# Optimization experiments

Measured on AMD Instinct MI355X. Metric: run time of the kernel, lower is better.

Reference implementation:

```python
import jax, jax.numpy as jnp
import numpy as np

N_QUBITS = 8
N_CYCLES = 4
N_LAYERS = 2  # log2(8) - 1
B = 65536

CNOT = jnp.array([[1, 0, 0, 0],
                  [0, 1, 0, 0],
                  [0, 0, 0, 1],
                  [0, 0, 1, 0]], dtype=jnp.complex64)


def apply_gate(state, U, wires):
    """Apply a (2^k x 2^k) gate U on the given wires of state (B, 2,2,...,2).
    Wire 0 is the leftmost (most significant) qubit axis."""
    k = len(wires)
    src = [w + 1 for w in wires]
    dst = list(range(1, 1 + k))
    st = jnp.moveaxis(state, src, dst)
    shp = st.shape
    st = st.reshape(shp[0], 2 ** k, -1)
    st = jnp.einsum('ij,bjr->bir', U, st)
    return jnp.moveaxis(st.reshape(shp), dst, src)


def apply_ry(state, q, angles):
    """Batched RY(angle) on qubit q; angles has shape (B,)."""
    st = jnp.moveaxis(state, q + 1, 1)  # (B, 2, rest...)
    c = jnp.cos(0.5 * angles).reshape((-1,) + (1,) * (st.ndim - 2))
    s = jnp.sin(0.5 * angles).reshape((-1,) + (1,) * (st.ndim - 2))
    s0, s1 = st[:, 0], st[:, 1]
    new = jnp.stack([c * s0 - s * s1, s * s0 + c * s1], axis=1)
    return jnp.moveaxis(new, 1, q + 1)


def crx_mat(theta):
    c = (jnp.cos(0.5 * theta) + 0j).astype(jnp.complex64)
    s = (-1j * jnp.sin(0.5 * theta)).astype(jnp.complex64)
    one = jnp.ones((), jnp.complex64)
    zero = jnp.zeros((), jnp.complex64)
    return jnp.stack([
        jnp.stack([one, zero, zero, zero]),
        jnp.stack([zero, one, zero, zero]),
        jnp.stack([zero, zero, c, s]),
        jnp.stack([zero, zero, s, c]),
    ])


def u3_mat(p):
    th, ph, lm = p[0], p[1], p[2]
    ct = (jnp.cos(0.5 * th) + 0j).astype(jnp.complex64)
    st = (jnp.sin(0.5 * th) + 0j).astype(jnp.complex64)
    el = jnp.exp(1j * lm).astype(jnp.complex64)
    ep = jnp.exp(1j * ph).astype(jnp.complex64)
    return jnp.stack([
        jnp.stack([ct, -el * st]),
        jnp.stack([ep * st, ep * el * ct]),
    ])


def expval_z(state, q):
    st = jnp.moveaxis(state, q + 1, 1)
    p = (st.real ** 2 + st.imag ** 2).reshape(st.shape[0], 2, -1).sum(-1)
    return p[:, 0] - p[:, 1]


def _forward(x, crx_theta, u3_params, w1, b1, w2, b2):
    b = x.shape[0]
    # |0...0> initial state, shape (B, 2,2,...,2)
    state = jnp.zeros((b, 2 ** N_QUBITS), jnp.complex64).at[:, 0].set(1.0)
    state = state.reshape((b,) + (2,) * N_QUBITS)
    # encoder: data re-uploading RY angle encoding + CNOT ring, n_cycles times
    for _ in range(N_CYCLES):
        for q in range(N_QUBITS):
            state = apply_ry(state, q, x[:, q])
        for q in range(N_QUBITS):
            state = apply_gate(state, CNOT, [q, (q + 1) % N_QUBITS])
    # QCNN conv/pool layers with shared weights per layer
    active = list(range(N_QUBITS))
    for layer in range(N_LAYERS):
        U = crx_mat(crx_theta[layer])
        for i in range(0, len(active) - 1, 2):
            state = apply_gate(state, U, [active[i], active[i + 1]])
        for i in range(1, len(active) - 1, 2):
            state = apply_gate(state, U, [active[i], active[i + 1]])
        remain = active[1::2]
        # mid-circuit expval in the original is discarded and does not alter state
        V = u3_mat(u3_params[layer])
        for q in remain:
            state = apply_gate(state, V, [q])
        active = remain
    feats = jnp.stack([expval_z(state, q) for q in active], axis=1)  # (B, 2)
    h = jnp.tanh(feats @ w1 + b1)
    return jax.nn.sigmoid(h @ w2 + b2)  # (B, 1)


def setup_inputs() -> dict:
    key = jax.random.key(0)
    ks = jax.random.split(key, 6)
    return {
        'x': jax.random.normal(ks[0], (B, N_QUBITS), jnp.float32),
        'crx_theta': jax.random.normal(ks[1], (N_LAYERS,), jnp.float32),
        'u3_params': jax.random.normal(ks[2], (N_LAYERS, 3), jnp.float32),
        'w1': jax.random.normal(ks[3], (2, 10), jnp.float32) * 0.5,
        'b1': jnp.zeros((10,), jnp.float32),
        'w2': jax.random.normal(ks[4], (10, 1), jnp.float32) * 0.5,
        'b2': jnp.zeros((1,), jnp.float32),
    }


def reference(x, crx_theta, u3_params, w1, b1, w2, b2):
    return _forward(x, crx_theta, u3_params, w1, b1, w2, b2)
```

## Files before the change

### kernel.cpp

```cpp
#include <hip/hip_runtime.h>


#define NQ 8
#define NE 2
typedef _Float16 h2 __attribute__((ext_vector_type(2)));

__device__ __forceinline__ float h2f(h2 v){ return __builtin_bit_cast(float, v); }
__device__ __forceinline__ h2 f2h(float v){ return __builtin_bit_cast(h2, v); }
__device__ __forceinline__ h2 u2h(unsigned u){ return __builtin_bit_cast(h2, u); }
__device__ __forceinline__ unsigned h2u(h2 v){ return __builtin_bit_cast(unsigned, v); }
__device__ __forceinline__ h2 negh(h2 v){ return u2h(h2u(v) ^ 0x80008000u); }
__device__ __forceinline__ h2 mk(float x){ return __builtin_bit_cast(h2, __builtin_amdgcn_cvt_pkrtz(x,x)); }
__device__ __forceinline__ h2 mk2(float a, float b){ return __builtin_bit_cast(h2, __builtin_amdgcn_cvt_pkrtz(a,b)); }
__device__ __forceinline__ h2 fma2h(h2 a, h2 b, h2 c){ return __builtin_elementwise_fma(a,b,c); }
__device__ __forceinline__ h2 swp(h2 v){ return __builtin_shufflevector(v,v,1,0); }
__device__ __forceinline__ h2 permh(h2 a, h2 b, unsigned sel){
    return u2h(__builtin_amdgcn_perm(h2u(a), h2u(b), sel));
}

template<int CTRL>
__device__ __forceinline__ float dppf(float v){
    return __int_as_float(__builtin_amdgcn_mov_dpp(__float_as_int(v), CTRL, 0xF, 0xF, true));
}
template<int M>
__device__ __forceinline__ float sx(float v){
    if constexpr (M==1)       return dppf<0xB1>(v);
    else if constexpr (M==2)  return dppf<0x4E>(v);
    else if constexpr (M==32) return __shfl_xor(v, 32, 64);
    else return __int_as_float(__builtin_amdgcn_ds_swizzle(__float_as_int(v), (M<<10)|0x1F));
}
__device__ __forceinline__ void cmulh(h2&R, h2&I, h2 C, h2 S, h2 nS){
    h2 nR = fma2h(C, R, nS*I);
    I = fma2h(C, I, S*R);
    R = nR;
}

#define FOR_E _Pragma("unroll") for (int e = 0; e < NE; ++e)

__global__ void qcnn_prep(const float* __restrict__ crx,
                          const float* __restrict__ u3p,
                          unsigned* __restrict__ ws){
    if (threadIdx.x==0 && blockIdx.x==0){
        auto PK=[](float lo, float hi)->unsigned{
            unsigned a=__builtin_bit_cast(unsigned short,(_Float16)lo);
            unsigned b=__builtin_bit_cast(unsigned short,(_Float16)hi);
            return a | (b<<16);
        };
        float sc0,cc0,sc1,cc1;
        __sincosf(0.5f*crx[0],&sc0,&cc0);
        __sincosf(0.5f*crx[1],&sc1,&cc1);
        ws[0]=PK(cc0,cc0); ws[1]=PK(sc0,sc0); ws[2]=PK(cc1,cc1); ws[3]=PK(sc1,sc1);
        float th0=u3p[0], ph0=u3p[1], lm0=u3p[2];
        float ust0,uct0; __sincosf(0.5f*th0,&ust0,&uct0);
        ws[4]=PK(uct0,uct0); ws[5]=PK(ust0,ust0); ws[6]=PK(-ust0,-ust0); ws[7]=PK(-ust0,ust0);
        float th1=u3p[3], ph1=u3p[4], lm1=u3p[5];
        float ust1,uct1; __sincosf(0.5f*th1,&ust1,&uct1);
        float sl1,cl1;   __sincosf(lm1,&sl1,&cl1);
        float sp1,cp1;   __sincosf(ph1,&sp1,&cp1);
        ws[8]=PK(uct1,uct1); ws[9]=PK(ust1,ust1); ws[10]=PK(-ust1,-ust1);
        ws[11]=PK(cl1,cl1); ws[12]=PK(sl1,sl1); ws[13]=PK(cp1,cp1); ws[14]=PK(sp1,sp1);
        float cpl1=cp1*cl1-sp1*sl1, spl1=sp1*cl1+cp1*sl1;
        float u01r=-ust1*cl1, u01i=-ust1*sl1;
        float u10r= ust1*cp1, u10i= ust1*sp1;
        float u11r= uct1*cpl1, u11i= uct1*spl1;
        ws[15]=PK(uct1,u11r); ws[16]=PK(u01r,u10r); ws[17]=PK(0.f,-u11i);
        ws[18]=PK(-u01i,-u10i); ws[19]=PK(0.f,u11i); ws[20]=PK(u01i,u10i);
        for(int k=0;k<4;++k){
            float kf=(float)k, sA,cA,sB,cB,sA2,cA2,sB2,cB2;
            __sincosf(lm0*kf,      &sA,&cA);
            __sincosf(lm0*(kf+1.f),&sB,&cB);
            __sincosf(ph0*kf,      &sA2,&cA2);
            __sincosf(ph0*(kf+1.f),&sB2,&cB2);
            unsigned* q = ws + 24 + k*4;
            q[0]=PK(cA,cB); q[1]=PK(sA,sB); q[2]=PK(cA2,cB2); q[3]=PK(sA2,sB2);
        }
    }
}

__global__ __launch_bounds__(256) void qcnn_kernel(
    const float* __restrict__ x,
    const unsigned* __restrict__ wsu,
    const float* __restrict__ w1,
    const float* __restrict__ b1,
    const float* __restrict__ w2,
    const float* __restrict__ b2,
    float* __restrict__ out,
    int Btot)
{
    const int gtid = blockIdx.x*256 + threadIdx.x;
    const int wv = gtid >> 6;
    const int l = threadIdx.x & 63;
    const int e0 = wv * NE;
    if (e0 >= Btot) return;
    const bool L5=(l>>5)&1, L4=(l>>4)&1, L3=(l>>3)&1, L2=(l>>2)&1, L1=(l>>1)&1, L0=l&1;

    const bool pb = __builtin_popcount(l) & 1;
    const int ba0 = (((l&32)|((l^(l>>1))&31)) << 2);
    const int ba1 = ba0 ^ (48<<2);

    const bool bits[6]={L5,L4,L3,L2,L1,L0};
    unsigned sm[6];
#pragma unroll
    for(int q=0;q<6;++q) sm[q] = bits[q] ? 0u : 0x80008000u;

    h2 cH[NE][6], tsH[NE][6];
    h2 c6h[NE], s6h[NE], ns6h[NE], c7h[NE], sv7h[NE];
    h2 A[NE], B[NE];
    FOR_E {
        const float4* xv = (const float4*)(x + (e0+e)*NQ);
        float4 xa=xv[0], xb=xv[1];
        float ang[8]={xa.x,xa.y,xa.z,xa.w,xb.x,xb.y,xb.z,xb.w};
        float cq[8], sq[8];
#pragma unroll
        for(int q=0;q<8;++q) __sincosf(0.5f*ang[q], &sq[q], &cq[q]);
#pragma unroll
        for(int q=0;q<6;++q){
            cH[e][q]=mk(cq[q]);
            tsH[e][q]=u2h(h2u(mk(sq[q])) ^ sm[q]);
        }
        c6h[e]=mk(cq[6]); s6h[e]=mk(sq[6]); ns6h[e]=negh(s6h[e]);
        c7h[e]=mk(cq[7]); sv7h[e]=mk2(-sq[7], sq[7]);
        float pl = (L5?sq[0]:cq[0])*(L4?sq[1]:cq[1])*(L3?sq[2]:cq[2])
                 * (L2?sq[3]:cq[3])*(L1?sq[4]:cq[4])*(L0?sq[5]:cq[5]);
        float pc6=pl*cq[6], ps6=pl*sq[6];
        A[e] = mk2(pc6*cq[7], pc6*sq[7]);
        B[e] = mk2(ps6*cq[7], ps6*sq[7]);
    }

    const h2 cc0h=u2h(wsu[0]), sn0h=u2h(wsu[1]), cc1h=u2h(wsu[2]), sn1h=u2h(wsu[3]);
    const h2 nsn0h=negh(sn0h), nsn1h=negh(sn1h);
    const h2 uct0h=u2h(wsu[4]), ust0h=u2h(wsu[5]), nust0h=u2h(wsu[6]), usv0h=u2h(wsu[7]);
    const h2 uct1h=u2h(wsu[8]), ust1h=u2h(wsu[9]), nust1h=u2h(wsu[10]);
    const h2 cl1h=u2h(wsu[11]), sl1h=u2h(wsu[12]), nsl1h=negh(sl1h);
    const h2 cp1h=u2h(wsu[13]), sp1h=u2h(wsu[14]), nsp1h=negh(sp1h);
    const h2 E0h=u2h(wsu[15]), E1h=u2h(wsu[16]), E2h=u2h(wsu[17]);
    const h2 E3h=u2h(wsu[18]), G2h=u2h(wsu[19]), G3h=u2h(wsu[20]);
    const int ki = (int)L4 + (int)L2 + (int)L0;
    uint4 dt = *(const uint4*)(wsu + 24 + ki*4);
    const h2 Clm=u2h(dt.x), Slm=u2h(dt.y), Cph=u2h(dt.z), Sph=u2h(dt.w);
    const h2 nSlm=negh(Slm), nSph=negh(Sph);
    const h2 tu1H = L4 ? ust0h : nust0h;
    const h2 tu3H = L2 ? ust0h : nust0h;
    const h2 tu5H = L0 ? ust0h : nust0h;

#define RY_L(q, M) do { FOR_E { \
    h2 oA = f2h(sx<M>(h2f(A[e]))), oB = f2h(sx<M>(h2f(B[e]))); \
    A[e] = fma2h(cH[e][q], A[e], tsH[e][q]*oA); \
    B[e] = fma2h(cH[e][q], B[e], tsH[e][q]*oB); } \
} while(0)

#define RINGF() do { FOR_E { \
    h2 TA = pb ? B[e] : A[e]; \
    h2 TS = pb ? A[e] : B[e]; \
    int V0 = (int)__builtin_amdgcn_perm(h2u(TS), h2u(TA), 0x07060100u); \
    int V1 = (int)__builtin_amdgcn_perm(h2u(TA), h2u(TS), 0x07060100u); \
    unsigned r0 = (unsigned)__builtin_amdgcn_ds_bpermute(ba0, V0); \
    unsigned r1 = (unsigned)__builtin_amdgcn_ds_bpermute(ba1, V1); \
    A[e] = u2h(__builtin_amdgcn_perm(r1, r0, 0x07060100u)); \
    B[e] = u2h(__builtin_amdgcn_perm(r1, r0, 0x05040302u)); } \
} while(0)

    RINGF();
#pragma unroll
    for(int cyc=0;cyc<3;++cyc){
        RY_L(0,32); RY_L(1,16); RY_L(2,8); RY_L(3,4); RY_L(4,2); RY_L(5,1);
        FOR_E { h2 nA = fma2h(c6h[e], A[e], ns6h[e]*B[e]);
                h2 nB = fma2h(s6h[e], A[e], c6h[e]*B[e]);
                A[e]=nA; B[e]=nB; }
        FOR_E { A[e] = fma2h(c7h[e], A[e], sv7h[e]*swp(A[e]));
                B[e] = fma2h(c7h[e], B[e], sv7h[e]*swp(B[e])); }
        RINGF();
    }

    h2 RA[NE], RB[NE], IA[NE], IB[NE];
    FOR_E { RA[e]=A[e]; RB[e]=B[e]; IA[e]=(h2){0,0}; IB[e]=(h2){0,0}; }

#define SHF4(M) h2 oRA[NE], oIA[NE], oRB[NE], oIB[NE]; \
    FOR_E { oRA[e]=f2h(sx<M>(h2f(RA[e]))); oIA[e]=f2h(sx<M>(h2f(IA[e]))); \
            oRB[e]=f2h(sx<M>(h2f(RB[e]))); oIB[e]=f2h(sx<M>(h2f(IB[e]))); }
#define CRX_LL(CSH, M, cc, sn, nsn) do { \
    const bool ct = (l >> (CSH)) & 1; \
    SHF4(M) \
    if (ct) { FOR_E { \
        RA[e] = fma2h(cc, RA[e], (sn)*oIA[e]); IA[e] = fma2h(cc, IA[e], (nsn)*oRA[e]); \
        RB[e] = fma2h(cc, RB[e], (sn)*oIB[e]); IB[e] = fma2h(cc, IB[e], (nsn)*oRB[e]); } } \
} while(0)
#define RYC0(M, T) do { \
    SHF4(M) \
    FOR_E { \
    RA[e] = fma2h(uct0h, RA[e], (T)*oRA[e]); IA[e] = fma2h(uct0h, IA[e], (T)*oIA[e]); \
    RB[e] = fma2h(uct0h, RB[e], (T)*oRB[e]); IB[e] = fma2h(uct0h, IB[e], (T)*oIB[e]); } \
} while(0)

    {   h2 oA[NE], oB[NE];
        FOR_E { oA[e]=f2h(sx<16>(h2f(RA[e]))); oB[e]=f2h(sx<16>(h2f(RB[e]))); }
        if (L5){ FOR_E {
            IA[e] = nsn0h*oA[e]; RA[e] = cc0h*RA[e];
            IB[e] = nsn0h*oB[e]; RB[e] = cc0h*RB[e]; } }
    }
    CRX_LL(3, 4, cc0h, sn0h, nsn0h);
    CRX_LL(1, 1, cc0h, sn0h, nsn0h);
    FOR_E {
        h2 oI = swp(IB[e]), oR = swp(RB[e]);
        RB[e] = fma2h(cc0h, RB[e], sn0h*oI);
        IB[e] = fma2h(cc0h, IB[e], nsn0h*oR);
    }
    CRX_LL(4, 8, cc0h, sn0h, nsn0h);
    CRX_LL(2, 2, cc0h, sn0h, nsn0h);
    if (L0) { FOR_E {
        h2 nRA = fma2h(cc0h, RA[e], sn0h*IB[e]);
        h2 nRB = fma2h(cc0h, RB[e], sn0h*IA[e]);
        h2 nIA = fma2h(cc0h, IA[e], nsn0h*RB[e]);
        h2 nIB = fma2h(cc0h, IB[e], nsn0h*RA[e]);
        RA[e]=nRA; RB[e]=nRB; IA[e]=nIA; IB[e]=nIB; } }
    FOR_E { cmulh(RA[e],IA[e],Clm,Slm,nSlm); cmulh(RB[e],IB[e],Clm,Slm,nSlm); }
    RYC0(16, tu1H);
    RYC0(4,  tu3H);
    RYC0(1,  tu5H);
    FOR_E {
        h2 sA=swp(RA[e]), sB=swp(RB[e]), tA=swp(IA[e]), tB=swp(IB[e]);
        RA[e] = fma2h(uct0h, RA[e], usv0h*sA); RB[e] = fma2h(uct0h, RB[e], usv0h*sB);
        IA[e] = fma2h(uct0h, IA[e], usv0h*tA); IB[e] = fma2h(uct0h, IB[e], usv0h*tB);
    }
    FOR_E { cmulh(RA[e],IA[e],Cph,Sph,nSph); cmulh(RB[e],IB[e],Cph,Sph,nSph); }

    CRX_LL(4, 4, cc1h, sn1h, nsn1h);
    if (L0) { FOR_E {
        h2 sIA=swp(IA[e]), sRA=swp(RA[e]), sIB=swp(IB[e]), sRB=swp(RB[e]);
        RA[e] = fma2h(cc1h, RA[e], sn1h*sIA); IA[e] = fma2h(cc1h, IA[e], nsn1h*sRA);
        RB[e] = fma2h(cc1h, RB[e], sn1h*sIB); IB[e] = fma2h(cc1h, IB[e], nsn1h*sRB); } }
    CRX_LL(2, 1, cc1h, sn1h, nsn1h);
    {
        if (L2){ FOR_E { cmulh(RA[e],IA[e],cl1h,sl1h,nsl1h); cmulh(RB[e],IB[e],cl1h,sl1h,nsl1h); } }
        h2 T = L2 ? ust1h : nust1h;
        SHF4(4)
        FOR_E {
            RA[e] = fma2h(uct1h, RA[e], T*oRA[e]); IA[e] = fma2h(uct1h, IA[e], T*oIA[e]);
            RB[e] = fma2h(uct1h, RB[e], T*oRB[e]); IB[e] = fma2h(uct1h, IB[e], T*oIB[e]);
        }
        if (L2){ FOR_E { cmulh(RA[e],IA[e],cp1h,sp1h,nsp1h); cmulh(RB[e],IB[e],cp1h,sp1h,nsp1h); } }
    }
    FOR_E {
        h2 sR=swp(RA[e]), sI=swp(IA[e]);
        h2 nR = fma2h(E3h,sI, fma2h(E2h,IA[e], fma2h(E1h,sR, E0h*RA[e])));
        h2 nI = fma2h(G3h,sR, fma2h(G2h,RA[e], fma2h(E1h,sI, E0h*IA[e])));
        RA[e]=nR; IA[e]=nI;
        h2 sR2=swp(RB[e]), sI2=swp(IB[e]);
        h2 nR2 = fma2h(E3h,sI2, fma2h(E2h,IB[e], fma2h(E1h,sR2, E0h*RB[e])));
        h2 nI2 = fma2h(G3h,sR2, fma2h(G2h,RB[e], fma2h(E1h,sI2, E0h*IB[e])));
        RB[e]=nR2; IB[e]=nI2;
    }

    float f0[NE], f1[NE];
    FOR_E {
        h2 P0 = permh(IA[e], RA[e], 0x05040100u);
        h2 P1 = permh(IA[e], RA[e], 0x07060302u);
        h2 P2 = permh(IB[e], RB[e], 0x05040100u);
        h2 P3 = permh(IB[e], RB[e], 0x07060302u);
        float q02 = __builtin_amdgcn_fdot2(P0, P0,
                      __builtin_amdgcn_fdot2(P2, P2, 0.0f, false), false);
        float q13 = __builtin_amdgcn_fdot2(P1, P1,
                      __builtin_amdgcn_fdot2(P3, P3, 0.0f, false), false);
        float tot = q02 + q13;
        f0[e] = L2 ? -tot : tot;
        f1[e] = q02 - q13;
    }

#define ROUTED_REDUCE(F, OUTV) do { \
    float u = L5 ? F[1] : F[0]; \
    float w = L5 ? F[0] : F[1]; \
    u += sx<32>(w); \
    u += sx<16>(u); u += sx<8>(u); u += sx<4>(u); u += sx<2>(u); u += sx<1>(u); \
    OUTV = u; \
} while(0)

    float F0, F1;
    ROUTED_REDUCE(f0, F0);
    ROUTED_REDUCE(f1, F1);

    const int k = l & 15;
    float contrib = 0.0f;
    if (k < 10) {
        float z = fmaf(F0, w1[k], fmaf(F1, w1[10+k], b1[k]));
        float ex = __expf(2.0f*z);
        contrib = ((ex-1.0f)/(ex+1.0f)) * w2[k];
    }
    contrib += sx<1>(contrib);
    contrib += sx<2>(contrib);
    contrib += sx<4>(contrib);
    contrib += sx<8>(contrib);
    if ((l & 31) == 0) {
        float a = contrib + b2[0];
        out[e0 + (l>>5)] = 1.0f/(1.0f + __expf(-a));
    }
}

extern "C" void kernel_launch(void* const* d_in, const int* in_sizes, int n_in,
                              void* d_out, int out_size, void* d_ws, size_t ws_size,
                              hipStream_t stream) {
    const float* x   = (const float*)d_in[0];
    const float* crx = (const float*)d_in[1];
    const float* u3p = (const float*)d_in[2];
    const float* w1  = (const float*)d_in[3];
    const float* b1  = (const float*)d_in[4];
    const float* w2  = (const float*)d_in[5];
    const float* b2  = (const float*)d_in[6];
    float* out = (float*)d_out;
    unsigned* ws = (unsigned*)d_ws;

    const int B = in_sizes[0] / NQ;
    hipLaunchKernelGGL(qcnn_prep, dim3(1), dim3(64), 0, stream, crx, u3p, ws);
    const int waves = (B + NE - 1) / NE;
    const int wavesPerBlock = 4;
    const int grid = (waves + wavesPerBlock - 1) / wavesPerBlock;
    hipLaunchKernelGGL(qcnn_kernel, dim3(grid), dim3(256), 0, stream,
                       x, ws, w1, b1, w2, b2, out, B);
}
```

Before: 117.5 us.

## Precompute data-independent second phase as unitary and apply via MFMA

The second circuit phase (CRX/U3 layers) does not depend on the input, so a prep kernel builds its 256x256 complex unitary by pushing basis states through it, then a second kernel repacks it into MFMA B-fragments. The main kernel runs the input-dependent RY/CRX cycles per element, stages the states in swizzled LDS, and multiplies them by the unitary with fp16 16x16x32 MFMAs, then reduces the Z expectations through shared memory. Blocks grow to 1024 threads covering 32 elements. This replaces the per-element shuffle-heavy gate sequence with a dense matmul, at the cost of two extra launches, a large workspace read, and more arithmetic per element.

```diff
diff --git a/kernel.cpp b/kernel.cpp
--- a/kernel.cpp
+++ b/kernel.cpp
@@ -3,7 +3,13 @@
 
 #define NQ 8
 #define NE 2
+#define FRAG_OFF 0
+#define UR_OFF   65536
+#define UI_OFF   98304
+
 typedef _Float16 h2 __attribute__((ext_vector_type(2)));
+typedef _Float16 h8 __attribute__((ext_vector_type(8)));
+typedef float    f4 __attribute__((ext_vector_type(4)));
 
 __device__ __forceinline__ float h2f(h2 v){ return __builtin_bit_cast(float, v); }
 __device__ __forceinline__ h2 f2h(float v){ return __builtin_bit_cast(h2, v); }
@@ -14,9 +20,6 @@
 __device__ __forceinline__ h2 mk2(float a, float b){ return __builtin_bit_cast(h2, __builtin_amdgcn_cvt_pkrtz(a,b)); }
 __device__ __forceinline__ h2 fma2h(h2 a, h2 b, h2 c){ return __builtin_elementwise_fma(a,b,c); }
 __device__ __forceinline__ h2 swp(h2 v){ return __builtin_shufflevector(v,v,1,0); }
-__device__ __forceinline__ h2 permh(h2 a, h2 b, unsigned sel){
-    return u2h(__builtin_amdgcn_perm(h2u(a), h2u(b), sel));
-}
 
 template<int CTRL>
 __device__ __forceinline__ float dppf(float v){
@@ -29,6 +32,9 @@
     else if constexpr (M==32) return __shfl_xor(v, 32, 64);
     else return __int_as_float(__builtin_amdgcn_ds_swizzle(__float_as_int(v), (M<<10)|0x1F));
 }
+__device__ __forceinline__ float bperm(int ba, float v){
+    return __int_as_float(__builtin_amdgcn_ds_bpermute(ba, __float_as_int(v)));
+}
 __device__ __forceinline__ void cmulh(h2&R, h2&I, h2 C, h2 S, h2 nS){
     h2 nR = fma2h(C, R, nS*I);
     I = fma2h(C, I, S*R);
@@ -36,118 +42,6 @@
 }
 
 #define FOR_E _Pragma("unroll") for (int e = 0; e < NE; ++e)
-
-__global__ void qcnn_prep(const float* __restrict__ crx,
-                          const float* __restrict__ u3p,
-                          unsigned* __restrict__ ws){
-    if (threadIdx.x==0 && blockIdx.x==0){
-        auto PK=[](float lo, float hi)->unsigned{
-            unsigned a=__builtin_bit_cast(unsigned short,(_Float16)lo);
-            unsigned b=__builtin_bit_cast(unsigned short,(_Float16)hi);
-            return a | (b<<16);
-        };
-        float sc0,cc0,sc1,cc1;
-        __sincosf(0.5f*crx[0],&sc0,&cc0);
-        __sincosf(0.5f*crx[1],&sc1,&cc1);
-        ws[0]=PK(cc0,cc0); ws[1]=PK(sc0,sc0); ws[2]=PK(cc1,cc1); ws[3]=PK(sc1,sc1);
-        float th0=u3p[0], ph0=u3p[1], lm0=u3p[2];
-        float ust0,uct0; __sincosf(0.5f*th0,&ust0,&uct0);
-        ws[4]=PK(uct0,uct0); ws[5]=PK(ust0,ust0); ws[6]=PK(-ust0,-ust0); ws[7]=PK(-ust0,ust0);
-        float th1=u3p[3], ph1=u3p[4], lm1=u3p[5];
-        float ust1,uct1; __sincosf(0.5f*th1,&ust1,&uct1);
-        float sl1,cl1;   __sincosf(lm1,&sl1,&cl1);
-        float sp1,cp1;   __sincosf(ph1,&sp1,&cp1);
-        ws[8]=PK(uct1,uct1); ws[9]=PK(ust1,ust1); ws[10]=PK(-ust1,-ust1);
-        ws[11]=PK(cl1,cl1); ws[12]=PK(sl1,sl1); ws[13]=PK(cp1,cp1); ws[14]=PK(sp1,sp1);
-        float cpl1=cp1*cl1-sp1*sl1, spl1=sp1*cl1+cp1*sl1;
-        float u01r=-ust1*cl1, u01i=-ust1*sl1;
-        float u10r= ust1*cp1, u10i= ust1*sp1;
-        float u11r= uct1*cpl1, u11i= uct1*spl1;
-        ws[15]=PK(uct1,u11r); ws[16]=PK(u01r,u10r); ws[17]=PK(0.f,-u11i);
-        ws[18]=PK(-u01i,-u10i); ws[19]=PK(0.f,u11i); ws[20]=PK(u01i,u10i);
-        for(int k=0;k<4;++k){
-            float kf=(float)k, sA,cA,sB,cB,sA2,cA2,sB2,cB2;
-            __sincosf(lm0*kf,      &sA,&cA);
-            __sincosf(lm0*(kf+1.f),&sB,&cB);
-            __sincosf(ph0*kf,      &sA2,&cA2);
-            __sincosf(ph0*(kf+1.f),&sB2,&cB2);
-            unsigned* q = ws + 24 + k*4;
-            q[0]=PK(cA,cB); q[1]=PK(sA,sB); q[2]=PK(cA2,cB2); q[3]=PK(sA2,sB2);
-        }
-    }
-}
-
-__global__ __launch_bounds__(256) void qcnn_kernel(
-    const float* __restrict__ x,
-    const unsigned* __restrict__ wsu,
-    const float* __restrict__ w1,
-    const float* __restrict__ b1,
-    const float* __restrict__ w2,
-    const float* __restrict__ b2,
-    float* __restrict__ out,
-    int Btot)
-{
-    const int gtid = blockIdx.x*256 + threadIdx.x;
-    const int wv = gtid >> 6;
-    const int l = threadIdx.x & 63;
-    const int e0 = wv * NE;
-    if (e0 >= Btot) return;
-    const bool L5=(l>>5)&1, L4=(l>>4)&1, L3=(l>>3)&1, L2=(l>>2)&1, L1=(l>>1)&1, L0=l&1;
-
-    const bool pb = __builtin_popcount(l) & 1;
-    const int ba0 = (((l&32)|((l^(l>>1))&31)) << 2);
-    const int ba1 = ba0 ^ (48<<2);
-
-    const bool bits[6]={L5,L4,L3,L2,L1,L0};
-    unsigned sm[6];
-#pragma unroll
-    for(int q=0;q<6;++q) sm[q] = bits[q] ? 0u : 0x80008000u;
-
-    h2 cH[NE][6], tsH[NE][6];
-    h2 c6h[NE], s6h[NE], ns6h[NE], c7h[NE], sv7h[NE];
-    h2 A[NE], B[NE];
-    FOR_E {
-        const float4* xv = (const float4*)(x + (e0+e)*NQ);
-        float4 xa=xv[0], xb=xv[1];
-        float ang[8]={xa.x,xa.y,xa.z,xa.w,xb.x,xb.y,xb.z,xb.w};
-        float cq[8], sq[8];
-#pragma unroll
-        for(int q=0;q<8;++q) __sincosf(0.5f*ang[q], &sq[q], &cq[q]);
-#pragma unroll
-        for(int q=0;q<6;++q){
-            cH[e][q]=mk(cq[q]);
-            tsH[e][q]=u2h(h2u(mk(sq[q])) ^ sm[q]);
-        }
-        c6h[e]=mk(cq[6]); s6h[e]=mk(sq[6]); ns6h[e]=negh(s6h[e]);
-        c7h[e]=mk(cq[7]); sv7h[e]=mk2(-sq[7], sq[7]);
-        float pl = (L5?sq[0]:cq[0])*(L4?sq[1]:cq[1])*(L3?sq[2]:cq[2])
-                 * (L2?sq[3]:cq[3])*(L1?sq[4]:cq[4])*(L0?sq[5]:cq[5]);
-        float pc6=pl*cq[6], ps6=pl*sq[6];
-        A[e] = mk2(pc6*cq[7], pc6*sq[7]);
-        B[e] = mk2(ps6*cq[7], ps6*sq[7]);
-    }
-
-    const h2 cc0h=u2h(wsu[0]), sn0h=u2h(wsu[1]), cc1h=u2h(wsu[2]), sn1h=u2h(wsu[3]);
-    const h2 nsn0h=negh(sn0h), nsn1h=negh(sn1h);
-    const h2 uct0h=u2h(wsu[4]), ust0h=u2h(wsu[5]), nust0h=u2h(wsu[6]), usv0h=u2h(wsu[7]);
-    const h2 uct1h=u2h(wsu[8]), ust1h=u2h(wsu[9]), nust1h=u2h(wsu[10]);
-    const h2 cl1h=u2h(wsu[11]), sl1h=u2h(wsu[12]), nsl1h=negh(sl1h);
-    const h2 cp1h=u2h(wsu[13]), sp1h=u2h(wsu[14]), nsp1h=negh(sp1h);
-    const h2 E0h=u2h(wsu[15]), E1h=u2h(wsu[16]), E2h=u2h(wsu[17]);
-    const h2 E3h=u2h(wsu[18]), G2h=u2h(wsu[19]), G3h=u2h(wsu[20]);
-    const int ki = (int)L4 + (int)L2 + (int)L0;
-    uint4 dt = *(const uint4*)(wsu + 24 + ki*4);
-    const h2 Clm=u2h(dt.x), Slm=u2h(dt.y), Cph=u2h(dt.z), Sph=u2h(dt.w);
-    const h2 nSlm=negh(Slm), nSph=negh(Sph);
-    const h2 tu1H = L4 ? ust0h : nust0h;
-    const h2 tu3H = L2 ? ust0h : nust0h;
-    const h2 tu5H = L0 ? ust0h : nust0h;
-
-#define RY_L(q, M) do { FOR_E { \
-    h2 oA = f2h(sx<M>(h2f(A[e]))), oB = f2h(sx<M>(h2f(B[e]))); \
-    A[e] = fma2h(cH[e][q], A[e], tsH[e][q]*oA); \
-    B[e] = fma2h(cH[e][q], B[e], tsH[e][q]*oB); } \
-} while(0)
 
 #define RINGF() do { FOR_E { \
     h2 TA = pb ? B[e] : A[e]; \
@@ -160,20 +54,36 @@
     B[e] = u2h(__builtin_amdgcn_perm(r1, r0, 0x05040302u)); } \
 } while(0)
 
-    RINGF();
-#pragma unroll
-    for(int cyc=0;cyc<3;++cyc){
-        RY_L(0,32); RY_L(1,16); RY_L(2,8); RY_L(3,4); RY_L(4,2); RY_L(5,1);
-        FOR_E { h2 nA = fma2h(c6h[e], A[e], ns6h[e]*B[e]);
-                h2 nB = fma2h(s6h[e], A[e], c6h[e]*B[e]);
-                A[e]=nA; B[e]=nB; }
-        FOR_E { A[e] = fma2h(c7h[e], A[e], sv7h[e]*swp(A[e]));
-                B[e] = fma2h(c7h[e], B[e], sv7h[e]*swp(B[e])); }
-        RINGF();
-    }
-
-    h2 RA[NE], RB[NE], IA[NE], IB[NE];
-    FOR_E { RA[e]=A[e]; RB[e]=B[e]; IA[e]=(h2){0,0}; IB[e]=(h2){0,0}; }
+struct P2C {
+    h2 cc0,sn0,nsn0, cc1,sn1,nsn1;
+    h2 uct0,ust0,nust0,usv0;
+    h2 uct1,ust1,nust1;
+    h2 cl1,sl1,nsl1, cp1,sp1,nsp1;
+    h2 E0,E1,E2,E3,G2,G3;
+    h2 Clm,Slm,nSlm,Cph,Sph,nSph;
+    h2 tu1,tu3,tu5;
+};
+
+__device__ __forceinline__ P2C load_consts(const unsigned* wsu, int l){
+    P2C K;
+    const bool L4=(l>>4)&1, L2=(l>>2)&1, L0=l&1;
+    K.cc0=u2h(wsu[0]); K.sn0=u2h(wsu[1]); K.cc1=u2h(wsu[2]); K.sn1=u2h(wsu[3]);
+    K.nsn0=negh(K.sn0); K.nsn1=negh(K.sn1);
+    K.uct0=u2h(wsu[4]); K.ust0=u2h(wsu[5]); K.nust0=u2h(wsu[6]); K.usv0=u2h(wsu[7]);
+    K.uct1=u2h(wsu[8]); K.ust1=u2h(wsu[9]); K.nust1=u2h(wsu[10]);
+    K.cl1=u2h(wsu[11]); K.sl1=u2h(wsu[12]); K.nsl1=negh(K.sl1);
+    K.cp1=u2h(wsu[13]); K.sp1=u2h(wsu[14]); K.nsp1=negh(K.sp1);
+    K.E0=u2h(wsu[15]); K.E1=u2h(wsu[16]); K.E2=u2h(wsu[17]);
+    K.E3=u2h(wsu[18]); K.G2=u2h(wsu[19]); K.G3=u2h(wsu[20]);
+    const int ki = (int)L4 + (int)L2 + (int)L0;
+    K.Clm=u2h(wsu[24+ki*4+0]); K.Slm=u2h(wsu[24+ki*4+1]);
+    K.Cph=u2h(wsu[24+ki*4+2]); K.Sph=u2h(wsu[24+ki*4+3]);
+    K.nSlm=negh(K.Slm); K.nSph=negh(K.Sph);
+    K.tu1 = L4 ? K.ust0 : K.nust0;
+    K.tu3 = L2 ? K.ust0 : K.nust0;
+    K.tu5 = L0 ? K.ust0 : K.nust0;
+    return K;
+}
 
 #define SHF4(M) h2 oRA[NE], oIA[NE], oRB[NE], oIB[NE]; \
     FOR_E { oRA[e]=f2h(sx<M>(h2f(RA[e]))); oIA[e]=f2h(sx<M>(h2f(IA[e]))); \
@@ -188,110 +98,315 @@
 #define RYC0(M, T) do { \
     SHF4(M) \
     FOR_E { \
-    RA[e] = fma2h(uct0h, RA[e], (T)*oRA[e]); IA[e] = fma2h(uct0h, IA[e], (T)*oIA[e]); \
-    RB[e] = fma2h(uct0h, RB[e], (T)*oRB[e]); IB[e] = fma2h(uct0h, IB[e], (T)*oIB[e]); } \
+    RA[e] = fma2h(K.uct0, RA[e], (T)*oRA[e]); IA[e] = fma2h(K.uct0, IA[e], (T)*oIA[e]); \
+    RB[e] = fma2h(K.uct0, RB[e], (T)*oRB[e]); IB[e] = fma2h(K.uct0, IB[e], (T)*oIB[e]); } \
 } while(0)
+
+__device__ __forceinline__ void phase2run(const int l, const P2C& K,
+    const h2* A, const h2* B, h2* RA, h2* RB, h2* IA, h2* IB)
+{
+    const bool L5=(l>>5)&1, L2=(l>>2)&1, L0=l&1;
+    FOR_E { RA[e]=A[e]; RB[e]=B[e]; IA[e]=(h2){0,0}; IB[e]=(h2){0,0}; }
 
     {   h2 oA[NE], oB[NE];
         FOR_E { oA[e]=f2h(sx<16>(h2f(RA[e]))); oB[e]=f2h(sx<16>(h2f(RB[e]))); }
         if (L5){ FOR_E {
-            IA[e] = nsn0h*oA[e]; RA[e] = cc0h*RA[e];
-            IB[e] = nsn0h*oB[e]; RB[e] = cc0h*RB[e]; } }
-    }
-    CRX_LL(3, 4, cc0h, sn0h, nsn0h);
-    CRX_LL(1, 1, cc0h, sn0h, nsn0h);
+            IA[e] = K.nsn0*oA[e]; RA[e] = K.cc0*RA[e];
+            IB[e] = K.nsn0*oB[e]; RB[e] = K.cc0*RB[e]; } }
+    }
+    CRX_LL(3, 4, K.cc0, K.sn0, K.nsn0);
+    CRX_LL(1, 1, K.cc0, K.sn0, K.nsn0);
     FOR_E {
         h2 oI = swp(IB[e]), oR = swp(RB[e]);
-        RB[e] = fma2h(cc0h, RB[e], sn0h*oI);
-        IB[e] = fma2h(cc0h, IB[e], nsn0h*oR);
-    }
-    CRX_LL(4, 8, cc0h, sn0h, nsn0h);
-    CRX_LL(2, 2, cc0h, sn0h, nsn0h);
+        RB[e] = fma2h(K.cc0, RB[e], K.sn0*oI);
+        IB[e] = fma2h(K.cc0, IB[e], K.nsn0*oR);
+    }
+    CRX_LL(4, 8, K.cc0, K.sn0, K.nsn0);
+    CRX_LL(2, 2, K.cc0, K.sn0, K.nsn0);
     if (L0) { FOR_E {
-        h2 nRA = fma2h(cc0h, RA[e], sn0h*IB[e]);
-        h2 nRB = fma2h(cc0h, RB[e], sn0h*IA[e]);
-        h2 nIA = fma2h(cc0h, IA[e], nsn0h*RB[e]);
-        h2 nIB = fma2h(cc0h, IB[e], nsn0h*RA[e]);
+        h2 nRA = fma2h(K.cc0, RA[e], K.sn0*IB[e]);
+        h2 nRB = fma2h(K.cc0, RB[e], K.sn0*IA[e]);
+        h2 nIA = fma2h(K.cc0, IA[e], K.nsn0*RB[e]);
+        h2 nIB = fma2h(K.cc0, IB[e], K.nsn0*RA[e]);
         RA[e]=nRA; RB[e]=nRB; IA[e]=nIA; IB[e]=nIB; } }
-    FOR_E { cmulh(RA[e],IA[e],Clm,Slm,nSlm); cmulh(RB[e],IB[e],Clm,Slm,nSlm); }
-    RYC0(16, tu1H);
-    RYC0(4,  tu3H);
-    RYC0(1,  tu5H);
+    FOR_E { cmulh(RA[e],IA[e],K.Clm,K.Slm,K.nSlm); cmulh(RB[e],IB[e],K.Clm,K.Slm,K.nSlm); }
+    RYC0(16, K.tu1);
+    RYC0(4,  K.tu3);
+    RYC0(1,  K.tu5);
     FOR_E {
         h2 sA=swp(RA[e]), sB=swp(RB[e]), tA=swp(IA[e]), tB=swp(IB[e]);
-        RA[e] = fma2h(uct0h, RA[e], usv0h*sA); RB[e] = fma2h(uct0h, RB[e], usv0h*sB);
-        IA[e] = fma2h(uct0h, IA[e], usv0h*tA); IB[e] = fma2h(uct0h, IB[e], usv0h*tB);
-    }
-    FOR_E { cmulh(RA[e],IA[e],Cph,Sph,nSph); cmulh(RB[e],IB[e],Cph,Sph,nSph); }
-
-    CRX_LL(4, 4, cc1h, sn1h, nsn1h);
+        RA[e] = fma2h(K.uct0, RA[e], K.usv0*sA); RB[e] = fma2h(K.uct0, RB[e], K.usv0*sB);
+        IA[e] = fma2h(K.uct0, IA[e], K.usv0*tA); IB[e] = fma2h(K.uct0, IB[e], K.usv0*tB);
+    }
+    FOR_E { cmulh(RA[e],IA[e],K.Cph,K.Sph,K.nSph); cmulh(RB[e],IB[e],K.Cph,K.Sph,K.nSph); }
+
+    CRX_LL(4, 4, K.cc1, K.sn1, K.nsn1);
     if (L0) { FOR_E {
         h2 sIA=swp(IA[e]), sRA=swp(RA[e]), sIB=swp(IB[e]), sRB=swp(RB[e]);
-        RA[e] = fma2h(cc1h, RA[e], sn1h*sIA); IA[e] = fma2h(cc1h, IA[e], nsn1h*sRA);
-        RB[e] = fma2h(cc1h, RB[e], sn1h*sIB); IB[e] = fma2h(cc1h, IB[e], nsn1h*sRB); } }
-    CRX_LL(2, 1, cc1h, sn1h, nsn1h);
+        RA[e] = fma2h(K.cc1, RA[e], K.sn1*sIA); IA[e] = fma2h(K.cc1, IA[e], K.nsn1*sRA);
+        RB[e] = fma2h(K.cc1, RB[e], K.sn1*sIB); IB[e] = fma2h(K.cc1, IB[e], K.nsn1*sRB); } }
+    CRX_LL(2, 1, K.cc1, K.sn1, K.nsn1);
     {
-        if (L2){ FOR_E { cmulh(RA[e],IA[e],cl1h,sl1h,nsl1h); cmulh(RB[e],IB[e],cl1h,sl1h,nsl1h); } }
-        h2 T = L2 ? ust1h : nust1h;
+        if (L2){ FOR_E { cmulh(RA[e],IA[e],K.cl1,K.sl1,K.nsl1); cmulh(RB[e],IB[e],K.cl1,K.sl1,K.nsl1); } }
+        h2 T = L2 ? K.ust1 : K.nust1;
         SHF4(4)
         FOR_E {
-            RA[e] = fma2h(uct1h, RA[e], T*oRA[e]); IA[e] = fma2h(uct1h, IA[e], T*oIA[e]);
-            RB[e] = fma2h(uct1h, RB[e], T*oRB[e]); IB[e] = fma2h(uct1h, IB[e], T*oIB[e]);
-        }
-        if (L2){ FOR_E { cmulh(RA[e],IA[e],cp1h,sp1h,nsp1h); cmulh(RB[e],IB[e],cp1h,sp1h,nsp1h); } }
+            RA[e] = fma2h(K.uct1, RA[e], T*oRA[e]); IA[e] = fma2h(K.uct1, IA[e], T*oIA[e]);
+            RB[e] = fma2h(K.uct1, RB[e], T*oRB[e]); IB[e] = fma2h(K.uct1, IB[e], T*oIB[e]);
+        }
+        if (L2){ FOR_E { cmulh(RA[e],IA[e],K.cp1,K.sp1,K.nsp1); cmulh(RB[e],IB[e],K.cp1,K.sp1,K.nsp1); } }
     }
     FOR_E {
         h2 sR=swp(RA[e]), sI=swp(IA[e]);
-        h2 nR = fma2h(E3h,sI, fma2h(E2h,IA[e], fma2h(E1h,sR, E0h*RA[e])));
-        h2 nI = fma2h(G3h,sR, fma2h(G2h,RA[e], fma2h(E1h,sI, E0h*IA[e])));
+        h2 nR = fma2h(K.E3,sI, fma2h(K.E2,IA[e], fma2h(K.E1,sR, K.E0*RA[e])));
+        h2 nI = fma2h(K.G3,sR, fma2h(K.G2,RA[e], fma2h(K.E1,sI, K.E0*IA[e])));
         RA[e]=nR; IA[e]=nI;
         h2 sR2=swp(RB[e]), sI2=swp(IB[e]);
-        h2 nR2 = fma2h(E3h,sI2, fma2h(E2h,IB[e], fma2h(E1h,sR2, E0h*RB[e])));
-        h2 nI2 = fma2h(G3h,sR2, fma2h(G2h,RB[e], fma2h(E1h,sI2, E0h*IB[e])));
+        h2 nR2 = fma2h(K.E3,sI2, fma2h(K.E2,IB[e], fma2h(K.E1,sR2, K.E0*RB[e])));
+        h2 nI2 = fma2h(K.G3,sR2, fma2h(K.G2,RB[e], fma2h(K.E1,sI2, K.E0*IB[e])));
         RB[e]=nR2; IB[e]=nI2;
     }
-
-    float f0[NE], f1[NE];
+}
+
+__global__ __launch_bounds__(1024) void qcnn_prep_u(
+    const float* __restrict__ crx, const float* __restrict__ u3p,
+    unsigned* __restrict__ ws)
+{
+    __shared__ unsigned cws[48];
+    if (threadIdx.x == 0){
+        auto PK=[](float lo, float hi)->unsigned{
+            unsigned a=__builtin_bit_cast(unsigned short,(_Float16)lo);
+            unsigned b=__builtin_bit_cast(unsigned short,(_Float16)hi);
+            return a | (b<<16);
+        };
+        float sc0,cc0,sc1,cc1;
+        __sincosf(0.5f*crx[0],&sc0,&cc0);
+        __sincosf(0.5f*crx[1],&sc1,&cc1);
+        cws[0]=PK(cc0,cc0); cws[1]=PK(sc0,sc0); cws[2]=PK(cc1,cc1); cws[3]=PK(sc1,sc1);
+        float th0=u3p[0], ph0=u3p[1], lm0=u3p[2];
+        float ust0,uct0; __sincosf(0.5f*th0,&ust0,&uct0);
+        cws[4]=PK(uct0,uct0); cws[5]=PK(ust0,ust0); cws[6]=PK(-ust0,-ust0); cws[7]=PK(-ust0,ust0);
+        float th1=u3p[3], ph1=u3p[4], lm1=u3p[5];
+        float ust1,uct1; __sincosf(0.5f*th1,&ust1,&uct1);
+        float sl1,cl1;   __sincosf(lm1,&sl1,&cl1);
+        float sp1,cp1;   __sincosf(ph1,&sp1,&cp1);
+        cws[8]=PK(uct1,uct1); cws[9]=PK(ust1,ust1); cws[10]=PK(-ust1,-ust1);
+        cws[11]=PK(cl1,cl1); cws[12]=PK(sl1,sl1); cws[13]=PK(cp1,cp1); cws[14]=PK(sp1,sp1);
+        float cpl1=cp1*cl1-sp1*sl1, spl1=sp1*cl1+cp1*sl1;
+        float u01r=-ust1*cl1, u01i=-ust1*sl1;
+        float u10r= ust1*cp1, u10i= ust1*sp1;
+        float u11r= uct1*cpl1, u11i= uct1*spl1;
+        cws[15]=PK(uct1,u11r); cws[16]=PK(u01r,u10r); cws[17]=PK(0.f,-u11i);
+        cws[18]=PK(-u01i,-u10i); cws[19]=PK(0.f,u11i); cws[20]=PK(u01i,u10i);
+        for(int k=0;k<4;++k){
+            float kf=(float)k, sA,cA,sB,cB,sA2,cA2,sB2,cB2;
+            __sincosf(lm0*kf,      &sA,&cA);
+            __sincosf(lm0*(kf+1.f),&sB,&cB);
+            __sincosf(ph0*kf,      &sA2,&cA2);
+            __sincosf(ph0*(kf+1.f),&sB2,&cB2);
+            unsigned* q = cws + 24 + k*4;
+            q[0]=PK(cA,cB); q[1]=PK(sA,sB); q[2]=PK(cA2,cB2); q[3]=PK(sA2,sB2);
+        }
+    }
+    __syncthreads();
+
+    const int l = threadIdx.x & 63;
+    const int w = threadIdx.x >> 6;
+    const P2C K = load_consts(cws, l);
+    const bool pb = __builtin_popcount(l) & 1;
+    const int ba0 = (((l&32)|((l^(l>>1))&31)) << 2);
+    const int ba1 = ba0 ^ (48<<2);
+
+    for (int it = 0; it < 8; ++it){
+        const int j0 = w*16 + it*2;
+        h2 A[NE], B[NE];
+        FOR_E {
+            A[e]=(h2){0,0}; B[e]=(h2){0,0};
+            const int j = j0 + e;
+            if (l == (j >> 2)){
+                const int slot = j & 3;
+                const _Float16 one = (_Float16)1.f;
+                if      (slot==0) A[e].x = one;
+                else if (slot==1) A[e].y = one;
+                else if (slot==2) B[e].x = one;
+                else              B[e].y = one;
+            }
+        }
+        RINGF();
+        h2 RA[NE], RB[NE], IA[NE], IB[NE];
+        phase2run(l, K, A, B, RA, RB, IA, IB);
+        FOR_E {
+            const int j = j0 + e;
+            *(uint2*)(ws + UR_OFF + j*128 + l*2) = make_uint2(h2u(RA[e]), h2u(RB[e]));
+            *(uint2*)(ws + UI_OFF + j*128 + l*2) = make_uint2(h2u(IA[e]), h2u(IB[e]));
+        }
+    }
+}
+
+__global__ void qcnn_prep_frag(unsigned* __restrict__ ws){
+    const int T = blockIdx.x*256 + threadIdx.x;
+    const int chunk = T >> 6, l = T & 63;
+    const int ct = chunk >> 4, ri = (chunk >> 3) & 1, ks = chunk & 7;
+    const unsigned short* U = (const unsigned short*)(ws + (ri ? UI_OFF : UR_OFF));
+    const int n = ct*16 + (l & 15);
+    const int g = l >> 4;
+    unsigned d[4];
+#pragma unroll
+    for (int p = 0; p < 4; ++p){
+        const int k0 = ks*32 + g*8 + 2*p;
+        unsigned lo = U[k0*256 + n];
+        unsigned hi = U[(k0+1)*256 + n];
+        d[p] = lo | (hi << 16);
+    }
+    uint4 v; v.x=d[0]; v.y=d[1]; v.z=d[2]; v.w=d[3];
+    *(uint4*)(ws + FRAG_OFF + chunk*256 + l*4) = v;
+}
+
+__global__ __launch_bounds__(1024) void qcnn_kernel(
+    const float* __restrict__ x,
+    const unsigned* __restrict__ wsu,
+    const float* __restrict__ w1,
+    const float* __restrict__ b1,
+    const float* __restrict__ w2,
+    const float* __restrict__ b2,
+    float* __restrict__ out,
+    int Btot)
+{
+    __shared__ __align__(16) unsigned char Sl[32*512];
+    __shared__ float parts[16][2][32];
+    const int tid = threadIdx.x;
+    const int l = tid & 63;
+    const int w = tid >> 6;
+    const int eblk = blockIdx.x * 32;
+    const int e0 = eblk + w*NE;
+    const bool L5=(l>>5)&1, L4=(l>>4)&1, L3=(l>>3)&1, L2=(l>>2)&1, L1=(l>>1)&1, L0=l&1;
+
+    const bool pb = __builtin_popcount(l) & 1;
+    const int ba0 = (((l&32)|((l^(l>>1))&31)) << 2);
+    const int ba1 = ba0 ^ (48<<2);
+
+    const bool bits[6]={L5,L4,L3,L2,L1,L0};
+    unsigned sm[6];
+#pragma unroll
+    for(int q=0;q<6;++q) sm[q] = bits[q] ? 0u : 0x80008000u;
+
+    h2 cH[NE][6], tsH[NE][6];
+    h2 c6h[NE], s6h[NE], ns6h[NE], c7h[NE], sv7h[NE];
+    h2 A[NE], B[NE];
     FOR_E {
-        h2 P0 = permh(IA[e], RA[e], 0x05040100u);
-        h2 P1 = permh(IA[e], RA[e], 0x07060302u);
-        h2 P2 = permh(IB[e], RB[e], 0x05040100u);
-        h2 P3 = permh(IB[e], RB[e], 0x07060302u);
-        float q02 = __builtin_amdgcn_fdot2(P0, P0,
-                      __builtin_amdgcn_fdot2(P2, P2, 0.0f, false), false);
-        float q13 = __builtin_amdgcn_fdot2(P1, P1,
-                      __builtin_amdgcn_fdot2(P3, P3, 0.0f, false), false);
-        float tot = q02 + q13;
-        f0[e] = L2 ? -tot : tot;
-        f1[e] = q02 - q13;
-    }
-
-#define ROUTED_REDUCE(F, OUTV) do { \
-    float u = L5 ? F[1] : F[0]; \
-    float w = L5 ? F[0] : F[1]; \
-    u += sx<32>(w); \
-    u += sx<16>(u); u += sx<8>(u); u += sx<4>(u); u += sx<2>(u); u += sx<1>(u); \
-    OUTV = u; \
+        const int ee = (e0 + e < Btot) ? (e0 + e) : (Btot - 1);
+        const float4* xv = (const float4*)(x + ee*NQ);
+        float4 xa=xv[0], xb=xv[1];
+        float ang[8]={xa.x,xa.y,xa.z,xa.w,xb.x,xb.y,xb.z,xb.w};
+        float cq[8], sq[8];
+#pragma unroll
+        for(int q=0;q<8;++q) __sincosf(0.5f*ang[q], &sq[q], &cq[q]);
+#pragma unroll
+        for(int q=0;q<6;++q){
+            cH[e][q]=mk(cq[q]);
+            tsH[e][q]=u2h(h2u(mk(sq[q])) ^ sm[q]);
+        }
+        c6h[e]=mk(cq[6]); s6h[e]=mk(sq[6]); ns6h[e]=negh(s6h[e]);
+        c7h[e]=mk(cq[7]); sv7h[e]=mk2(-sq[7], sq[7]);
+        float pl = (L5?sq[0]:cq[0])*(L4?sq[1]:cq[1])*(L3?sq[2]:cq[2])
+                 * (L2?sq[3]:cq[3])*(L1?sq[4]:cq[4])*(L0?sq[5]:cq[5]);
+        float pc6=pl*cq[6], ps6=pl*sq[6];
+        A[e] = mk2(pc6*cq[7], pc6*sq[7]);
+        B[e] = mk2(ps6*cq[7], ps6*sq[7]);
+    }
+
+#define RY_L(q, M) do { FOR_E { \
+    h2 oA = f2h(sx<M>(h2f(A[e]))), oB = f2h(sx<M>(h2f(B[e]))); \
+    A[e] = fma2h(cH[e][q], A[e], tsH[e][q]*oA); \
+    B[e] = fma2h(cH[e][q], B[e], tsH[e][q]*oB); } \
 } while(0)
 
-    float F0, F1;
-    ROUTED_REDUCE(f0, F0);
-    ROUTED_REDUCE(f1, F1);
-
-    const int k = l & 15;
-    float contrib = 0.0f;
-    if (k < 10) {
-        float z = fmaf(F0, w1[k], fmaf(F1, w1[10+k], b1[k]));
-        float ex = __expf(2.0f*z);
-        contrib = ((ex-1.0f)/(ex+1.0f)) * w2[k];
-    }
-    contrib += sx<1>(contrib);
-    contrib += sx<2>(contrib);
-    contrib += sx<4>(contrib);
-    contrib += sx<8>(contrib);
-    if ((l & 31) == 0) {
-        float a = contrib + b2[0];
-        out[e0 + (l>>5)] = 1.0f/(1.0f + __expf(-a));
+    RINGF();
+#pragma unroll
+    for(int cyc=0;cyc<3;++cyc){
+        RY_L(0,32); RY_L(1,16); RY_L(2,8); RY_L(3,4); RY_L(4,2); RY_L(5,1);
+        FOR_E { h2 nA = fma2h(c6h[e], A[e], ns6h[e]*B[e]);
+                h2 nB = fma2h(s6h[e], A[e], c6h[e]*B[e]);
+                A[e]=nA; B[e]=nB; }
+        FOR_E { A[e] = fma2h(c7h[e], A[e], sv7h[e]*swp(A[e]));
+                B[e] = fma2h(c7h[e], B[e], sv7h[e]*swp(B[e])); }
+        if (cyc < 2) RINGF();
+    }
+
+    FOR_E {
+        const int r = w*NE + e;
+        const unsigned off = ((unsigned)(r*512 + l*8)) ^ (((unsigned)(r&7))<<4);
+        *(uint2*)(Sl + off) = make_uint2(h2u(A[e]), h2u(B[e]));
+    }
+    __syncthreads();
+
+    f4 aR0={0,0,0,0}, aI0={0,0,0,0}, aR1={0,0,0,0}, aI1={0,0,0,0};
+    const int m0 = l & 15, g = l >> 4;
+    const unsigned swzA = ((unsigned)(m0 & 7)) << 4;
+    const unsigned* frag = wsu + FRAG_OFF;
+#pragma unroll
+    for (int ks = 0; ks < 8; ++ks){
+        const unsigned c = (unsigned)(ks*64 + g*16);
+        h8 a0 = *(const h8*)(Sl + (((unsigned)(m0*512)        + c) ^ swzA));
+        h8 a1 = *(const h8*)(Sl + (((unsigned)((m0+16)*512)   + c) ^ swzA));
+        h8 br = *(const h8*)(frag + (w*16 +     ks)*256 + l*4);
+        h8 bi = *(const h8*)(frag + (w*16 + 8 + ks)*256 + l*4);
+        aR0 = __builtin_amdgcn_mfma_f32_16x16x32_f16(a0, br, aR0, 0, 0, 0);
+        aR1 = __builtin_amdgcn_mfma_f32_16x16x32_f16(a1, br, aR1, 0, 0, 0);
+        aI0 = __builtin_amdgcn_mfma_f32_16x16x32_f16(a0, bi, aI0, 0, 0, 0);
+        aI1 = __builtin_amdgcn_mfma_f32_16x16x32_f16(a1, bi, aI1, 0, 0, 0);
+    }
+
+    const float s3 = (w & 1) ? -1.f : 1.f;
+    const float s7 = (l & 1) ? -1.f : 1.f;
+    float f0a[4], f1a[4], f0b[4], f1b[4];
+#pragma unroll
+    for (int r = 0; r < 4; ++r){
+        float nv0 = fmaf(aR0[r], aR0[r], aI0[r]*aI0[r]);
+        float nv1 = fmaf(aR1[r], aR1[r], aI1[r]*aI1[r]);
+        f0a[r] = s3*nv0; f1a[r] = s7*nv0;
+        f0b[r] = s3*nv1; f1b[r] = s7*nv1;
+    }
+#pragma unroll
+    for (int r = 0; r < 4; ++r){
+        f0a[r] += sx<1>(f0a[r]); f0a[r] += sx<2>(f0a[r]); f0a[r] += sx<4>(f0a[r]); f0a[r] += sx<8>(f0a[r]);
+        f1a[r] += sx<1>(f1a[r]); f1a[r] += sx<2>(f1a[r]); f1a[r] += sx<4>(f1a[r]); f1a[r] += sx<8>(f1a[r]);
+        f0b[r] += sx<1>(f0b[r]); f0b[r] += sx<2>(f0b[r]); f0b[r] += sx<4>(f0b[r]); f0b[r] += sx<8>(f0b[r]);
+        f1b[r] += sx<1>(f1b[r]); f1b[r] += sx<2>(f1b[r]); f1b[r] += sx<4>(f1b[r]); f1b[r] += sx<8>(f1b[r]);
+    }
+    if ((l & 15) == 0){
+        const int rb = g*4;
+#pragma unroll
+        for (int r = 0; r < 4; ++r){
+            parts[w][0][rb+r]    = f0a[r];
+            parts[w][1][rb+r]    = f1a[r];
+            parts[w][0][16+rb+r] = f0b[r];
+            parts[w][1][16+rb+r] = f1b[r];
+        }
+    }
+    __syncthreads();
+
+    if (tid < 512){
+        const int elem = tid >> 4, k = tid & 15;
+        float F0 = 0.f, F1 = 0.f;
+#pragma unroll
+        for (int ww = 0; ww < 16; ++ww){
+            F0 += parts[ww][0][elem];
+            F1 += parts[ww][1][elem];
+        }
+        float contrib = 0.0f;
+        if (k < 10){
+            float z = fmaf(F0, w1[k], fmaf(F1, w1[10+k], b1[k]));
+            float ex = __expf(2.0f*z);
+            contrib = ((ex-1.0f)/(ex+1.0f)) * w2[k];
+        }
+        contrib += sx<1>(contrib);
+        contrib += sx<2>(contrib);
+        contrib += sx<4>(contrib);
+        contrib += sx<8>(contrib);
+        if (k == 0 && eblk + elem < Btot){
+            out[eblk + elem] = 1.0f/(1.0f + __expf(-(contrib + b2[0])));
+        }
     }
 }
 
@@ -309,10 +424,9 @@
     unsigned* ws = (unsigned*)d_ws;
 
     const int B = in_sizes[0] / NQ;
-    hipLaunchKernelGGL(qcnn_prep, dim3(1), dim3(64), 0, stream, crx, u3p, ws);
-    const int waves = (B + NE - 1) / NE;
-    const int wavesPerBlock = 4;
-    const int grid = (waves + wavesPerBlock - 1) / wavesPerBlock;
-    hipLaunchKernelGGL(qcnn_kernel, dim3(grid), dim3(256), 0, stream,
+    hipLaunchKernelGGL(qcnn_prep_u,    dim3(1),  dim3(1024), 0, stream, crx, u3p, ws);
+    hipLaunchKernelGGL(qcnn_prep_frag, dim3(64), dim3(256),  0, stream, ws);
+    const int grid = (B + 31) / 32;
+    hipLaunchKernelGGL(qcnn_kernel, dim3(grid), dim3(1024), 0, stream,
                        x, ws, w1, b1, w2, b2, out, B);
 }
```

Measured after the change: 138.5 us. 1.18x slower.
